# Kernel tuning notes

Measured on AMD Instinct MI355X. Metric: run time of the kernel, lower is better.

## Reference

```python
import jax, jax.numpy as jnp
import numpy as np


def setup_inputs() -> dict:
    key = jax.random.key(0)
    k1, k2, k3 = jax.random.split(key, 3)
    B, C, L = 4, 64, 4096
    proj_query = jax.random.normal(k1, (B, C, L), dtype=jnp.float32)
    proj_key = jax.random.normal(k2, (B, C, L), dtype=jnp.float32)
    proj_val = jax.random.normal(k3, (B, C, L), dtype=jnp.float32)
    padding_mask = jnp.ones((B, 1, L), dtype=jnp.float32)
    return {
        "proj_query": proj_query,
        "proj_key": proj_key,
        "proj_val": proj_val,
        "padding_mask": padding_mask,
    }


def reference(proj_query, proj_key, proj_val, padding_mask):
    # proj_query/key/val: [B, C, L]; padding_mask: [B, 1, L]
    B, C, L1 = proj_query.shape
    scale = 1.0 / np.sqrt(C).astype(np.float32)
    # energy[b, lq, lk] = sum_c q[b,c,lq] * k[b,c,lk]
    energy = jnp.einsum("bcq,bck->bqk", proj_query, proj_key)
    attention = energy * scale + jnp.log(padding_mask + 1e-6)  # mask broadcasts over lq
    attention = jax.nn.softmax(attention, axis=-1) * padding_mask
    attention_t = jnp.transpose(attention, (0, 2, 1))  # [B, lk, lq]
    # out[b, c, lq] = sum_lk v[b,c,lk] * attention_t[b,lk,lq]
    out = jnp.einsum("bck,bkq->bcq", proj_val, attention_t)
    return out, attention_t
```

## Files before the change

### kernel.cpp

```cpp
#include <hip/hip_runtime.h>
#include <stdint.h>

#define BB 4
#define CCH 64
#define LLEN 4096
#define QS2 0.18033688011112042f
#define TQ 64
#define TK 64
#define NCHUNK 8
#define TPC 8
#define NTB 256

typedef __bf16 bf16;
typedef bf16 bf16x4 __attribute__((ext_vector_type(4)));
typedef bf16 bf16x8 __attribute__((ext_vector_type(8)));
typedef float f32x4 __attribute__((ext_vector_type(4)));

#define EXP2F(x) __builtin_amdgcn_exp2f(x)
#define LOG2F(x) __builtin_amdgcn_logf(x)

__device__ __forceinline__ int swz(int row, int col) {
    return row * 64 + (col ^ ((row & 7) << 3));
}

__device__ __forceinline__ void g2l16(const void* g, void* l) {
    __builtin_amdgcn_global_load_lds(
        (const __attribute__((address_space(1))) void*)g,
        (__attribute__((address_space(3))) void*)l, 16, 0, 0);
}

#define WAITVM0 asm volatile("s_waitcnt vmcnt(0)" ::: "memory")
#define WAITVM16 asm volatile("s_waitcnt vmcnt(16)" ::: "memory")
#define WAITLGKM0 asm volatile("s_waitcnt lgkmcnt(0)" ::: "memory")
#define BAR() __builtin_amdgcn_s_barrier()
#define PRIO(n) __builtin_amdgcn_s_setprio(n)

__device__ __forceinline__ void stage_rows(const bf16* src, bf16* dst, int w, int l) {
#pragma unroll
    for (int i = 0; i < 2; ++i) {
        int ci = w * 2 + i;
        g2l16(src + ci * 512 + l * 8, dst + ci * 512);
    }
}

__global__ __launch_bounds__(NTB) void prep_all(
    const float* __restrict__ qg, const float* __restrict__ kg,
    const float* __restrict__ vg, const float* __restrict__ mg,
    bf16* __restrict__ qT, bf16* __restrict__ kT,
    bf16* __restrict__ vF, float* __restrict__ wS, float* __restrict__ wE)
{
    const int tid = threadIdx.x;
    if (blockIdx.x < 512) {
        __shared__ float t[64][65];
        const int isK = blockIdx.x >> 8;
        const int idx = blockIdx.x & 255;
        const int b = idx >> 6;
        const int lt = idx & 63;
        const float* src = (isK ? kg : qg) + (size_t)b * CCH * LLEN + lt * 64;
        bf16* dst = (isK ? kT : qT) + ((size_t)b * LLEN + lt * 64) * 64;

        int c = tid >> 2, x0 = (tid & 3) * 16;
#pragma unroll
        for (int j = 0; j < 4; ++j) {
            float4 f = *(const float4*)&src[(size_t)c * LLEN + x0 + j * 4];
            t[c][x0 + j * 4 + 0] = f.x;
            t[c][x0 + j * 4 + 1] = f.y;
            t[c][x0 + j * 4 + 2] = f.z;
            t[c][x0 + j * 4 + 3] = f.w;
        }
        __syncthreads();
        int lk = tid >> 2;
        int g0 = (tid & 3) * 2;
#pragma unroll
        for (int gi = 0; gi < 2; ++gi) {
            int gg = g0 + gi;
            bf16x8 v;
#pragma unroll
            for (int j = 0; j < 8; ++j) v[j] = (bf16)t[gg * 8 + j][lk];
            *(bf16x8*)&dst[lk * 64 + ((gg ^ (lk & 7)) * 8)] = v;
        }
    } else if (blockIdx.x < 768) {
        const int row = blockIdx.x - 512;
        const int b = row >> 6;
        const int c = row & 63;
        const int mt = c >> 4, cl = c & 15;
        const size_t base = (size_t)row * LLEN;
        const int x0 = tid * 16;
        const int tile = x0 >> 6;
        float f[16];
#pragma unroll
        for (int j = 0; j < 4; ++j) {
            float4 v4 = *(const float4*)&vg[base + x0 + j * 4];
            f[j * 4 + 0] = v4.x; f[j * 4 + 1] = v4.y;
            f[j * 4 + 2] = v4.z; f[j * 4 + 3] = v4.w;
        }
        bf16* vFb = vF + (size_t)(b * 64 + tile) * 4096;
#pragma unroll
        for (int k2 = 0; k2 < 4; ++k2) {
            int rem = (x0 & 63) + 4 * k2;
            int s = rem >> 5, hl = (rem >> 4) & 1, g = (rem >> 2) & 3;
            bf16x4 hv = {(bf16)f[4 * k2 + 0], (bf16)f[4 * k2 + 1],
                         (bf16)f[4 * k2 + 2], (bf16)f[4 * k2 + 3]};
            *(bf16x4*)&vFb[(size_t)(((s * 4 + mt) * 64 + 16 * g + cl) * 8 + hl * 4)] = hv;
        }
    } else {
        const int b = blockIdx.x - 768;
        int x0 = tid * 16;
#pragma unroll
        for (int j = 0; j < 16; ++j) {
            float m = mg[(size_t)b * LLEN + x0 + j];
            float w = m + 1e-6f;
            wS[(size_t)b * LLEN + x0 + j] = LOG2F(w);
            wE[(size_t)b * LLEN + x0 + j] = LOG2F(w * m);
        }
    }
}

__global__ __launch_bounds__(NTB) void attn_stats(
    const bf16* __restrict__ qT, const bf16* __restrict__ kT,
    const float* __restrict__ wS, float* __restrict__ sums,
    float* __restrict__ outp)
{
    __shared__ __align__(16) bf16 kbuf[2][TK * CCH];
    __shared__ __align__(16) float wbuf[2][TK];
    __shared__ float red[4][TQ];

    const int tid = threadIdx.x;
    const int l = tid & 63;
    const int w = tid >> 6;
    const int g = l >> 4;
    const int cl = l & 15;

    const int idx = blockIdx.x;
    const int chunk = idx & 7;
    const int lqt = (idx >> 3) & 63;
    const int b = idx >> 9;
    const int lq0 = lqt * TQ;
    const size_t bL = (size_t)b * LLEN;

    {
        size_t o = ((size_t)idx * NTB + tid) * 2;
        *(float2*)&outp[o] = make_float2(0.f, 0.f);
    }

    stage_rows(qT + (bL + lq0) * 64, kbuf[1], w, l);
    stage_rows(kT + (bL + chunk * 512) * 64, kbuf[0], w, l);
    if (w == 0 && l < 16) g2l16(wS + bL + chunk * 512 + l * 4, wbuf[0]);
    WAITVM0;
    BAR();
    bf16x8 qf[4][2];
#pragma unroll
    for (int strip = 0; strip < 4; ++strip) {
        qf[strip][0] = *(const bf16x8*)&kbuf[1][swz(strip * 16 + cl, 8 * g)];
        qf[strip][1] = *(const bf16x8*)&kbuf[1][swz(strip * 16 + cl, 32 + 8 * g)];
    }
    WAITLGKM0;
    BAR();

    float sacc[4] = {0.f, 0.f, 0.f, 0.f};
#pragma unroll
    for (int it = 0; it < TPC; ++it) {
        const int kcur = it & 1;
        const int lk0 = chunk * 512 + it * 64;

        if (it < TPC - 1) {
            stage_rows(kT + (bL + lk0 + 64) * 64, kbuf[kcur ^ 1], w, l);
            if (w == 0 && l < 16) g2l16(wS + bL + lk0 + 64 + l * 4, wbuf[kcur ^ 1]);
        }

        bf16x8 kf0 = *(const bf16x8*)&kbuf[kcur][swz(16 * w + cl, 8 * g)];
        bf16x8 kf1 = *(const bf16x8*)&kbuf[kcur][swz(16 * w + cl, 32 + 8 * g)];
        float4 wv = *(const float4*)&wbuf[kcur][16 * w + 4 * g];

        PRIO(1);
#pragma unroll
        for (int strip = 0; strip < 4; ++strip) {
            f32x4 e = (f32x4){0.f, 0.f, 0.f, 0.f};
            e = __builtin_amdgcn_mfma_f32_16x16x32_bf16(kf0, qf[strip][0], e, 0, 0, 0);
            e = __builtin_amdgcn_mfma_f32_16x16x32_bf16(kf1, qf[strip][1], e, 0, 0, 0);
            sacc[strip] += EXP2F(fmaf(e[0], QS2, wv.x));
            sacc[strip] += EXP2F(fmaf(e[1], QS2, wv.y));
            sacc[strip] += EXP2F(fmaf(e[2], QS2, wv.z));
            sacc[strip] += EXP2F(fmaf(e[3], QS2, wv.w));
        }
        PRIO(0);

        if (it < TPC - 1) {
            WAITVM0;
            WAITLGKM0;
            BAR();
        }
    }

#pragma unroll
    for (int strip = 0; strip < 4; ++strip) {
        sacc[strip] += __shfl_xor(sacc[strip], 16);
        sacc[strip] += __shfl_xor(sacc[strip], 32);
    }
    if (l < 16) {
#pragma unroll
        for (int strip = 0; strip < 4; ++strip) red[w][strip * 16 + l] = sacc[strip];
    }
    __syncthreads();
    if (tid < TQ) {
        float s = red[0][tid] + red[1][tid] + red[2][tid] + red[3][tid];
        sums[(bL + lq0 + tid) * NCHUNK + chunk] = s;
    }
}

__global__ __launch_bounds__(NTB, 4) void attn_emit(
    const bf16* __restrict__ qT, const bf16* __restrict__ kT,
    const bf16* __restrict__ vF, const float* __restrict__ wE,
    const float* __restrict__ sums, float* __restrict__ outp,
    float* __restrict__ attnT)
{
    __shared__ __align__(16) bf16 kbuf[2][TK * CCH];
    __shared__ __align__(16) bf16 vbuf[2][TK * CCH];
    __shared__ __align__(16) float wbuf[2][TK];

    const int tid = threadIdx.x;
    const int l = tid & 63;
    const int w = tid >> 6;
    const int strip = w * 16;
    const int g = l >> 4;
    const int cl = l & 15;

    const int idx = blockIdx.x;
    const int chunk = idx & 7;
    const int lqt = (idx >> 3) & 63;
    const int b = idx >> 9;
    const int lq0 = lqt * TQ;
    const size_t bL = (size_t)b * LLEN;
    const size_t obase = (size_t)b * CCH * LLEN;

    stage_rows(qT + (bL + lq0) * 64, kbuf[0], w, l);
    stage_rows(kT + (bL + chunk * 512) * 64, kbuf[1], w, l);
    stage_rows(vF + (size_t)(b * 64 + chunk * 8) * 4096, vbuf[0], w, l);
    if (w == 0 && l < 16) g2l16(wE + bL + chunk * 512 + l * 4, wbuf[0]);

    float ls2;
    {
        const float4* sp = (const float4*)&sums[(bL + lq0 + strip + cl) * NCHUNK];
        float4 a = sp[0], c4 = sp[1];
        float ssum = ((a.x + a.y) + (a.z + a.w)) + ((c4.x + c4.y) + (c4.z + c4.w));
        ls2 = -LOG2F(ssum);
    }

    WAITVM0;
    BAR();
    bf16x8 qf0 = *(const bf16x8*)&kbuf[0][swz(strip + cl, 8 * g)];
    bf16x8 qf1 = *(const bf16x8*)&kbuf[0][swz(strip + cl, 32 + 8 * g)];
    WAITLGKM0;
    BAR();

    f32x4 o4[4];
#pragma unroll
    for (int t = 0; t < 4; ++t) o4[t] = (f32x4){0.f, 0.f, 0.f, 0.f};

#pragma unroll
    for (int it = 0; it < TPC; ++it) {
        const int kcur = (it & 1) ^ 1;
        const int vcur = it & 1;
        const int lk0 = chunk * 512 + it * 64;

        if (it < TPC - 1) {
            stage_rows(kT + (bL + lk0 + 64) * 64, kbuf[kcur ^ 1], w, l);
            stage_rows(vF + (size_t)(b * 64 + (lk0 >> 6) + 1) * 4096, vbuf[vcur ^ 1], w, l);
            if (w == 0 && l < 16) g2l16(wE + bL + lk0 + 64 + l * 4, wbuf[vcur ^ 1]);
        }

        f32x4 e4[4];
#pragma unroll
        for (int t = 0; t < 4; ++t) e4[t] = (f32x4){0.f, 0.f, 0.f, 0.f};
        PRIO(1);
#pragma unroll
        for (int t = 0; t < 4; ++t) {
            bf16x8 kf0 = *(const bf16x8*)&kbuf[kcur][swz(16 * t + cl, 8 * g)];
            e4[t] = __builtin_amdgcn_mfma_f32_16x16x32_bf16(kf0, qf0, e4[t], 0, 0, 0);
            bf16x8 kf1 = *(const bf16x8*)&kbuf[kcur][swz(16 * t + cl, 32 + 8 * g)];
            e4[t] = __builtin_amdgcn_mfma_f32_16x16x32_bf16(kf1, qf1, e4[t], 0, 0, 0);
        }
        PRIO(0);

        bf16x8 vf[8];
#pragma unroll
        for (int u = 0; u < 8; ++u)
            vf[u] = *(const bf16x8*)&vbuf[vcur][(u * 64 + l) * 8];

        float p[4][4];
#pragma unroll
        for (int t = 0; t < 4; ++t) {
            float4 wv = *(const float4*)&wbuf[vcur][16 * t + 4 * g];
            p[t][0] = EXP2F(fmaf(e4[t][0], QS2, ls2 + wv.x));
            p[t][1] = EXP2F(fmaf(e4[t][1], QS2, ls2 + wv.y));
            p[t][2] = EXP2F(fmaf(e4[t][2], QS2, ls2 + wv.z));
            p[t][3] = EXP2F(fmaf(e4[t][3], QS2, ls2 + wv.w));
        }

        bf16x8 pb[2];
#pragma unroll
        for (int s = 0; s < 2; ++s)
#pragma unroll
            for (int j = 0; j < 8; ++j)
                pb[s][j] = (bf16)p[2 * s + (j >> 2)][j & 3];
        PRIO(1);
#pragma unroll
        for (int s = 0; s < 2; ++s)
#pragma unroll
            for (int mt = 0; mt < 4; ++mt)
                o4[mt] = __builtin_amdgcn_mfma_f32_16x16x32_bf16(
                    vf[s * 4 + mt], pb[s], o4[mt], 0, 0, 0);
        PRIO(0);

#pragma unroll
        for (int t = 0; t < 4; ++t)
#pragma unroll
            for (int r = 0; r < 4; ++r) {
                int lkg = lk0 + 16 * t + 4 * g + r;
                attnT[(bL + lkg) * LLEN + lq0 + strip + cl] = p[t][r];
            }

        if (it < TPC - 1) {
            WAITVM16;
            WAITLGKM0;
            BAR();
        }
    }

#pragma unroll
    for (int mt = 0; mt < 4; ++mt)
#pragma unroll
        for (int r = 0; r < 4; ++r) {
            int c = 16 * mt + 4 * g + r;
            atomicAdd(&outp[obase + (size_t)c * LLEN + lq0 + strip + cl], o4[mt][r]);
        }
}

extern "C" void kernel_launch(void* const* d_in, const int* in_sizes, int n_in,
                              void* d_out, int out_size, void* d_ws, size_t ws_size,
                              hipStream_t stream) {
    const float* qg = (const float*)d_in[0];
    const float* kg = (const float*)d_in[1];
    const float* vg = (const float*)d_in[2];
    const float* mg = (const float*)d_in[3];
    float* outp = (float*)d_out;
    float* attnT = outp + (size_t)BB * CCH * LLEN;

    char* ws = (char*)d_ws;
    bf16* qT = (bf16*)ws;
    bf16* kT = (bf16*)(ws + (2u << 20));
    bf16* vF = (bf16*)(ws + (4u << 20));
    float* wS = (float*)(ws + (6u << 20));
    float* wE = (float*)(ws + (6u << 20) + (64u << 10));
    float* sums = (float*)(ws + (6u << 20) + (128u << 10));

    prep_all<<<772, NTB, 0, stream>>>(qg, kg, vg, mg, qT, kT, vF, wS, wE);
    attn_stats<<<BB * (LLEN / TQ) * NCHUNK, NTB, 0, stream>>>(qT, kT, wS, sums, outp);
    attn_emit<<<BB * (LLEN / TQ) * NCHUNK, NTB, 0, stream>>>(qT, kT, vF, wE, sums, outp, attnT);
}
```

Before: 99.79 us.

## Widen attn_emit blocks to 128 queries with 8 waves and fewer key chunks

```diff
diff --git a/kernel.cpp b/kernel.cpp
--- a/kernel.cpp
+++ b/kernel.cpp
@@ -10,6 +10,10 @@
 #define NCHUNK 8
 #define TPC 8
 #define NTB 256
+#define TQE 128
+#define NTE 512
+#define NCHE 4
+#define TPE 16
 
 typedef __bf16 bf16;
 typedef bf16 bf16x4 __attribute__((ext_vector_type(4)));
@@ -41,6 +45,9 @@
         int ci = w * 2 + i;
         g2l16(src + ci * 512 + l * 8, dst + ci * 512);
     }
+}
+__device__ __forceinline__ void stage_tile8(const bf16* src, bf16* dst, int w, int l) {
+    g2l16(src + w * 512 + l * 8, dst + w * 512);
 }
 
 __global__ __launch_bounds__(NTB) void prep_all(
@@ -208,7 +215,7 @@
     }
 }
 
-__global__ __launch_bounds__(NTB, 4) void attn_emit(
+__global__ __launch_bounds__(NTE, 4) void attn_emit(
     const bf16* __restrict__ qT, const bf16* __restrict__ kT,
     const bf16* __restrict__ vF, const float* __restrict__ wE,
     const float* __restrict__ sums, float* __restrict__ outp,
@@ -226,18 +233,15 @@
     const int cl = l & 15;
 
     const int idx = blockIdx.x;
-    const int chunk = idx & 7;
-    const int lqt = (idx >> 3) & 63;
-    const int b = idx >> 9;
-    const int lq0 = lqt * TQ;
+    const int chunk = idx & (NCHE - 1);
+    const int lqt = (idx >> 2) & 31;
+    const int b = idx >> 7;
+    const int lq0 = lqt * TQE;
     const size_t bL = (size_t)b * LLEN;
     const size_t obase = (size_t)b * CCH * LLEN;
-
-    stage_rows(qT + (bL + lq0) * 64, kbuf[0], w, l);
-    stage_rows(kT + (bL + chunk * 512) * 64, kbuf[1], w, l);
-    stage_rows(vF + (size_t)(b * 64 + chunk * 8) * 4096, vbuf[0], w, l);
-    if (w == 0 && l < 16) g2l16(wE + bL + chunk * 512 + l * 4, wbuf[0]);
-
+    bf16* kflat = &kbuf[0][0];
+
+    stage_rows(qT + (bL + lq0) * 64, kflat, w, l);
     float ls2;
     {
         const float4* sp = (const float4*)&sums[(bL + lq0 + strip + cl) * NCHUNK];
@@ -245,28 +249,35 @@
         float ssum = ((a.x + a.y) + (a.z + a.w)) + ((c4.x + c4.y) + (c4.z + c4.w));
         ls2 = -LOG2F(ssum);
     }
-
     WAITVM0;
     BAR();
-    bf16x8 qf0 = *(const bf16x8*)&kbuf[0][swz(strip + cl, 8 * g)];
-    bf16x8 qf1 = *(const bf16x8*)&kbuf[0][swz(strip + cl, 32 + 8 * g)];
+    bf16x8 qf0 = *(const bf16x8*)&kflat[swz(strip + cl, 8 * g)];
+    bf16x8 qf1 = *(const bf16x8*)&kflat[swz(strip + cl, 32 + 8 * g)];
     WAITLGKM0;
     BAR();
 
+    {
+        const int lk0 = chunk * (TPE * TK);
+        stage_tile8(kT + (bL + lk0) * 64, kbuf[0], w, l);
+        stage_tile8(vF + (size_t)(b * 64 + (lk0 >> 6)) * 4096, vbuf[0], w, l);
+        if (w == 0 && l < 16) g2l16(wE + bL + lk0 + l * 4, wbuf[0]);
+    }
+    WAITVM0;
+    BAR();
+
     f32x4 o4[4];
 #pragma unroll
     for (int t = 0; t < 4; ++t) o4[t] = (f32x4){0.f, 0.f, 0.f, 0.f};
 
 #pragma unroll
-    for (int it = 0; it < TPC; ++it) {
-        const int kcur = (it & 1) ^ 1;
-        const int vcur = it & 1;
-        const int lk0 = chunk * 512 + it * 64;
-
-        if (it < TPC - 1) {
-            stage_rows(kT + (bL + lk0 + 64) * 64, kbuf[kcur ^ 1], w, l);
-            stage_rows(vF + (size_t)(b * 64 + (lk0 >> 6) + 1) * 4096, vbuf[vcur ^ 1], w, l);
-            if (w == 0 && l < 16) g2l16(wE + bL + lk0 + 64 + l * 4, wbuf[vcur ^ 1]);
+    for (int it = 0; it < TPE; ++it) {
+        const int cur = it & 1;
+        const int lk0 = chunk * (TPE * TK) + it * 64;
+
+        if (it < TPE - 1) {
+            stage_tile8(kT + (bL + lk0 + 64) * 64, kbuf[cur ^ 1], w, l);
+            stage_tile8(vF + (size_t)(b * 64 + (lk0 >> 6) + 1) * 4096, vbuf[cur ^ 1], w, l);
+            if (w == 0 && l < 16) g2l16(wE + bL + lk0 + 64 + l * 4, wbuf[cur ^ 1]);
         }
 
         f32x4 e4[4];
@@ -275,22 +286,17 @@
         PRIO(1);
 #pragma unroll
         for (int t = 0; t < 4; ++t) {
-            bf16x8 kf0 = *(const bf16x8*)&kbuf[kcur][swz(16 * t + cl, 8 * g)];
+            bf16x8 kf0 = *(const bf16x8*)&kbuf[cur][swz(16 * t + cl, 8 * g)];
             e4[t] = __builtin_amdgcn_mfma_f32_16x16x32_bf16(kf0, qf0, e4[t], 0, 0, 0);
-            bf16x8 kf1 = *(const bf16x8*)&kbuf[kcur][swz(16 * t + cl, 32 + 8 * g)];
+            bf16x8 kf1 = *(const bf16x8*)&kbuf[cur][swz(16 * t + cl, 32 + 8 * g)];
             e4[t] = __builtin_amdgcn_mfma_f32_16x16x32_bf16(kf1, qf1, e4[t], 0, 0, 0);
         }
         PRIO(0);
 
-        bf16x8 vf[8];
-#pragma unroll
-        for (int u = 0; u < 8; ++u)
-            vf[u] = *(const bf16x8*)&vbuf[vcur][(u * 64 + l) * 8];
-
         float p[4][4];
 #pragma unroll
         for (int t = 0; t < 4; ++t) {
-            float4 wv = *(const float4*)&wbuf[vcur][16 * t + 4 * g];
+            float4 wv = *(const float4*)&wbuf[cur][16 * t + 4 * g];
             p[t][0] = EXP2F(fmaf(e4[t][0], QS2, ls2 + wv.x));
             p[t][1] = EXP2F(fmaf(e4[t][1], QS2, ls2 + wv.y));
             p[t][2] = EXP2F(fmaf(e4[t][2], QS2, ls2 + wv.z));
@@ -305,11 +311,16 @@
                 pb[s][j] = (bf16)p[2 * s + (j >> 2)][j & 3];
         PRIO(1);
 #pragma unroll
-        for (int s = 0; s < 2; ++s)
+        for (int s = 0; s < 2; ++s) {
+            bf16x8 vf4[4];
+#pragma unroll
+            for (int mt = 0; mt < 4; ++mt)
+                vf4[mt] = *(const bf16x8*)&vbuf[cur][((s * 4 + mt) * 64 + l) * 8];
 #pragma unroll
             for (int mt = 0; mt < 4; ++mt)
                 o4[mt] = __builtin_amdgcn_mfma_f32_16x16x32_bf16(
-                    vf[s * 4 + mt], pb[s], o4[mt], 0, 0, 0);
+                    vf4[mt], pb[s], o4[mt], 0, 0, 0);
+        }
         PRIO(0);
 
 #pragma unroll
@@ -320,7 +331,7 @@
                 attnT[(bL + lkg) * LLEN + lq0 + strip + cl] = p[t][r];
             }
 
-        if (it < TPC - 1) {
+        if (it < TPE - 1) {
             WAITVM16;
             WAITLGKM0;
             BAR();
@@ -356,5 +367,5 @@
 
     prep_all<<<772, NTB, 0, stream>>>(qg, kg, vg, mg, qT, kT, vF, wS, wE);
     attn_stats<<<BB * (LLEN / TQ) * NCHUNK, NTB, 0, stream>>>(qT, kT, wS, sums, outp);
-    attn_emit<<<BB * (LLEN / TQ) * NCHUNK, NTB, 0, stream>>>(qT, kT, vF, wE, sums, outp, attnT);
-}
+    attn_emit<<<BB * (LLEN / TQE) * NCHE, NTE, 0, stream>>>(qT, kT, vF, wE, sums, outp, attnT);
+}
```

Result: faster. 92.67 us, median of 2 (-7.1%).
